# Kernel tuning notes

Hardware: AMD Instinct MI355X
Metric: run time of the kernel (lower is better)

## Reference

```python
import jax, jax.numpy as jnp
import numpy as np

B, S, E, H, L = 16, 1024, 512, 8, 4
D = E // H  # head_dim = 64


def setup_inputs() -> dict:
    key = jax.random.key(0)
    ks = jax.random.split(key, 16)
    std = 0.02
    inp = {
        "q": jax.random.normal(ks[0], (B, S, E), jnp.float32),
        "k": jax.random.normal(ks[1], (B, S, E), jnp.float32),
        "v": jax.random.normal(ks[2], (B, S, E), jnp.float32),
        # standard Linear params (torch convention: W is (out, in))
        "Wq": jax.random.normal(ks[3], (E, E), jnp.float32) * std,
        "bq": jnp.zeros((E,), jnp.float32),
        "Wk": jax.random.normal(ks[4], (E, E), jnp.float32) * std,
        "bk": jnp.zeros((E,), jnp.float32),
        # WFLinear: shared weight elementwise-multiplied by per-language factor
        "Wv_share": jax.random.normal(ks[5], (E, E), jnp.float32) * std,
        "Wv_spec": 1.0 + jax.random.normal(ks[6], (L, E, E), jnp.float32) * std,
        "bv_share": jnp.zeros((E,), jnp.float32),
        "bv_spec": jax.random.normal(ks[7], (L, E), jnp.float32) * std,
        "Wo_share": jax.random.normal(ks[8], (E, E), jnp.float32) * std,
        "Wo_spec": 1.0 + jax.random.normal(ks[9], (L, E, E), jnp.float32) * std,
        "bo_share": jnp.zeros((E,), jnp.float32),
        "bo_spec": jax.random.normal(ks[10], (L, E), jnp.float32) * std,
        "mask": jax.random.randint(ks[11], (B, S), 0, 2, jnp.int32),
        "languageID": 1,
    }
    return inp


def reference(q, k, v, Wq, bq, Wk, bk, Wv_share, Wv_spec, bv_share, bv_spec,
              Wo_share, Wo_spec, bo_share, bo_spec, mask, languageID):
    scaling = D ** (-0.5)
    # projections (torch Linear: x @ W.T + b)
    Q = (q @ Wq.T + bq).reshape(B, S, H, D).transpose(0, 2, 1, 3) * scaling
    K = (k @ Wk.T + bk).reshape(B, S, H, D).transpose(0, 2, 1, 3)
    Wv = Wv_share * Wv_spec[languageID]
    bv = bv_share + bv_spec[languageID]
    V = (v @ Wv.T + bv).reshape(B, S, H, D).transpose(0, 2, 1, 3)
    # NOTE: faithful to original — Q already scaled by d_k^-0.5, and
    # AttentionWF divides by sqrt(d_k) AGAIN (effective scale 1/d_k).
    alpha = jnp.einsum("bhqd,bhkd->bhqk", Q, K) / np.float32(np.sqrt(D))
    m = (mask == 0)[:, None, None, :]  # (B,1,1,S) over key axis
    alpha = jnp.where(m, jnp.float32(-1e9), alpha)
    alpha = jax.nn.softmax(alpha, axis=-1)
    # dropout p=0.0 -> identity
    ctx = jnp.einsum("bhqk,bhkd->bhqd", alpha, V)  # (B,H,S,D)
    concat = ctx.transpose(0, 2, 1, 3).reshape(B, S, E)
    Wo = Wo_share * Wo_spec[languageID]
    bo = bo_share + bo_spec[languageID]
    return concat @ Wo.T + bo
```

## Files before the change

### kernel.cpp

```cpp
#include <hip/hip_runtime.h>

#define B_ 16
#define S_ 1024
#define E_ 512
#define H_ 8
#define D_ 64
#define L_ 4
#define M_ (B_*S_)

typedef unsigned short u16;
typedef __attribute__((ext_vector_type(8))) short bf16x8;
typedef __attribute__((ext_vector_type(4))) float f32x4;
typedef __attribute__((ext_vector_type(4))) unsigned uint4v;

__device__ __forceinline__ u16 f2bf(float x) {
  unsigned u = __float_as_uint(x);
  unsigned r = (u + 0x7fffu + ((u >> 16) & 1u)) >> 16;
  return (u16)r;
}
__device__ __forceinline__ ushort4 f2bf4(float4 f) {
  ushort4 u;
  u.x = f2bf(f.x); u.y = f2bf(f.y); u.z = f2bf(f.z); u.w = f2bf(f.w);
  return u;
}
__device__ __forceinline__ unsigned cvt_pk_bf16(float lo, float hi) {
  unsigned r;
  asm("v_cvt_pk_bf16_f32 %0, %1, %2" : "=v"(r) : "v"(lo), "v"(hi));
  return r;
}

typedef __attribute__((address_space(1))) const void gconst_void;
typedef __attribute__((address_space(3))) void lds_void;
__device__ __forceinline__ void gl_lds16(const void* g, void* l) {
  __builtin_amdgcn_global_load_lds((gconst_void*)g, (lds_void*)l, 16, 0, 0);
}
__device__ __forceinline__ void fence_vm0_barrier() {
  asm volatile("s_waitcnt vmcnt(0)" ::: "memory");
  __builtin_amdgcn_s_barrier();
}

__global__ __launch_bounds__(256) void prep_w(
    const float* __restrict__ Wq, const float* __restrict__ Wk,
    const float* __restrict__ Wv_sh, const float* __restrict__ Wv_sp,
    const float* __restrict__ Wo_sh, const float* __restrict__ Wo_sp,
    const float* __restrict__ bv_sh, const float* __restrict__ bv_sp,
    const float* __restrict__ bo_sh, const float* __restrict__ bo_sp,
    const int* __restrict__ langp,
    u16* __restrict__ Wq_b, u16* __restrict__ Wk_b,
    u16* __restrict__ Wv_b, u16* __restrict__ Wo_b,
    float* __restrict__ bv_f, float* __restrict__ bo_f) {
  int lang = langp[0];
  int i = blockIdx.x * 256 + threadIdx.x;
  size_t wofs = (size_t)lang * (E_*E_/4) + i;
  ((ushort4*)Wq_b)[i] = f2bf4(((const float4*)Wq)[i]);
  ((ushort4*)Wk_b)[i] = f2bf4(((const float4*)Wk)[i]);
  float4 vs = ((const float4*)Wv_sh)[i], vp = ((const float4*)Wv_sp)[wofs];
  float4 os = ((const float4*)Wo_sh)[i], op = ((const float4*)Wo_sp)[wofs];
  float4 vv = {vs.x*vp.x, vs.y*vp.y, vs.z*vp.z, vs.w*vp.w};
  float4 oo = {os.x*op.x, os.y*op.y, os.z*op.z, os.w*op.w};
  ((ushort4*)Wv_b)[i] = f2bf4(vv);
  ((ushort4*)Wo_b)[i] = f2bf4(oo);
  if (i < E_/4) {
    float4 b1 = ((const float4*)bv_sh)[i], b2 = ((const float4*)(bv_sp + (size_t)lang*E_))[i];
    float4 b3 = ((const float4*)bo_sh)[i], b4 = ((const float4*)(bo_sp + (size_t)lang*E_))[i];
    float4 r1 = {b1.x+b2.x, b1.y+b2.y, b1.z+b2.z, b1.w+b2.w};
    float4 r2 = {b3.x+b4.x, b3.y+b4.y, b3.z+b4.z, b3.w+b4.w};
    ((float4*)bv_f)[i] = r1;
    ((float4*)bo_f)[i] = r2;
  }
}

#define QBUF 4096
__global__ __launch_bounds__(256) void gemm_qkv(
    const float* __restrict__ q, const float* __restrict__ k, const float* __restrict__ v,
    const u16* __restrict__ Wq_b, const u16* __restrict__ Wk_b, const u16* __restrict__ Wv_b,
    const float* __restrict__ bq, const float* __restrict__ bk, const float* __restrict__ bv,
    u16* __restrict__ Qb, u16* __restrict__ Kb, u16* __restrict__ Vt) {
  __shared__ __align__(16) float sAfD[2*QBUF];
  __shared__ __align__(16) u16   sBD[2*QBUF];
  const int z = blockIdx.y;
  const float* A    = (z == 0) ? q : (z == 1) ? k : v;
  const u16*   Bw   = (z == 0) ? Wq_b : (z == 1) ? Wk_b : Wv_b;
  const float* bias = (z == 0) ? bq : (z == 1) ? bk : bv;
  const int t = threadIdx.x;
  const int hw = blockIdx.x;
  const int wk = (hw & 7) * 64 + (hw >> 3);
  const int m0 = (wk >> 2) * 128, n0 = (wk & 3) * 128;
  const int lane = t & 63, wid = t >> 6;
  const int m16 = lane & 15, qq = lane >> 4;
  const int wrow = (wid >> 1) * 64, wcol = (wid & 1) * 64;
  f32x4 acc[4][4] = {};
  const int ca0 = wid*4;
  const float* ap[4];
#pragma unroll
  for (int i = 0; i < 4; ++i)
    ap[i] = A + (size_t)(m0 + (ca0+i)*8 + (lane >> 3)) * E_ + (lane & 7) * 4;
  const int cb0 = wid*2, cb1 = wid*2 + 1;
  const u16* bp0 = Bw + (size_t)(n0 + cb0*16 + (lane >> 2)) * E_ + (lane & 3) * 8;
  const u16* bp1 = Bw + (size_t)(n0 + cb1*16 + (lane >> 2)) * E_ + (lane & 3) * 8;
  {
#pragma unroll
    for (int i = 0; i < 4; ++i) gl_lds16(ap[i], &sAfD[(ca0+i)*256]);
    gl_lds16(bp0, &sBD[cb0*512]);
    gl_lds16(bp1, &sBD[cb1*512]);
#pragma unroll
    for (int i = 0; i < 4; ++i) ap[i] += 32;
    bp0 += 32; bp1 += 32;
  }
  fence_vm0_barrier();
  for (int kt = 0; kt < 16; ++kt) {
    if (kt < 15) {
      float* sa = &sAfD[((kt+1)&1)*QBUF];
      u16*   sb = &sBD[((kt+1)&1)*QBUF];
#pragma unroll
      for (int i = 0; i < 4; ++i) gl_lds16(ap[i], sa + (ca0+i)*256);
      gl_lds16(bp0, sb + cb0*512);
      gl_lds16(bp1, sb + cb1*512);
#pragma unroll
      for (int i = 0; i < 4; ++i) ap[i] += 32;
      bp0 += 32; bp1 += 32;
    }
    const float* saf = &sAfD[(kt&1)*QBUF];
    const u16*   sbb = &sBD[(kt&1)*QBUF];
    bf16x8 af[4], bfm[4];
#pragma unroll
    for (int mt = 0; mt < 4; ++mt) {
      const float* ar = saf + (wrow + mt*16 + m16) * 32 + qq*8;
      f32x4 a0 = *(const f32x4*)ar;
      f32x4 a1 = *(const f32x4*)(ar + 4);
      union { uint4v u; bf16x8 h; } cv;
      cv.u = (uint4v){ cvt_pk_bf16(a0[0], a0[1]), cvt_pk_bf16(a0[2], a0[3]),
                       cvt_pk_bf16(a1[0], a1[1]), cvt_pk_bf16(a1[2], a1[3]) };
      af[mt] = cv.h;
    }
#pragma unroll
    for (int nt = 0; nt < 4; ++nt)
      bfm[nt] = *(const bf16x8*)(sbb + (wcol + nt*16 + m16) * 32 + qq*8);
#pragma unroll
    for (int mt = 0; mt < 4; ++mt)
#pragma unroll
      for (int nt = 0; nt < 4; ++nt)
        acc[mt][nt] = __builtin_amdgcn_mfma_f32_16x16x32_bf16(af[mt], bfm[nt], acc[mt][nt], 0, 0, 0);
    if (kt < 15) fence_vm0_barrier();
  }
  float bvv[4];
#pragma unroll
  for (int nt = 0; nt < 4; ++nt) bvv[nt] = bias[n0 + wcol + nt*16 + m16];
  if (z < 2) {
    u16* out = (z == 0) ? Qb : Kb;
#pragma unroll
    for (int mt = 0; mt < 4; ++mt) {
      int gm = m0 + wrow + mt*16 + qq*4;
#pragma unroll
      for (int nt = 0; nt < 4; ++nt) {
        int gn = n0 + wcol + nt*16 + m16;
#pragma unroll
        for (int r = 0; r < 4; ++r)
          out[(size_t)(gm + r) * E_ + gn] = f2bf(acc[mt][nt][r] + bvv[nt]);
      }
    }
  } else {
#pragma unroll
    for (int mt = 0; mt < 4; ++mt) {
      int tok0 = m0 + wrow + mt*16 + qq*4;
      int bb = tok0 >> 10, s0 = tok0 & 1023;
#pragma unroll
      for (int nt = 0; nt < 4; ++nt) {
        int dim = n0 + wcol + nt*16 + m16;
        uint2 wv = { cvt_pk_bf16(acc[mt][nt][0] + bvv[nt], acc[mt][nt][1] + bvv[nt]),
                     cvt_pk_bf16(acc[mt][nt][2] + bvv[nt], acc[mt][nt][3] + bvv[nt]) };
        *(uint2*)(Vt + ((size_t)(bb*E_ + dim))*S_ + s0) = wv;
      }
    }
  }
}

__global__ __launch_bounds__(256) void gemm_lds(
    const u16* __restrict__ A, const u16* __restrict__ Bw,
    const float* __restrict__ bias, float* __restrict__ out) {
  __shared__ __align__(16) u16 sAD[2*QBUF];
  __shared__ __align__(16) u16 sBD[2*QBUF];
  const int t = threadIdx.x;
  const int hw = blockIdx.x;
  const int wk = (hw & 7) * 64 + (hw >> 3);
  const int m0 = (wk >> 2) * 128, n0 = (wk & 3) * 128;
  const int lane = t & 63, wid = t >> 6;
  const int m16 = lane & 15, qq = lane >> 4;
  const int wrow = (wid >> 1) * 64, wcol = (wid & 1) * 64;
  f32x4 acc[4][4] = {};
  const int c0 = 2*wid, c1 = 2*wid + 1;
  const int colk = (lane & 3) * 8;
  const int r0 = c0*16 + (lane >> 2), r1 = c1*16 + (lane >> 2);
  const u16* a0 = A  + (size_t)(m0 + r0) * E_ + colk;
  const u16* a1 = A  + (size_t)(m0 + r1) * E_ + colk;
  const u16* b0 = Bw + (size_t)(n0 + r0) * E_ + colk;
  const u16* b1 = Bw + (size_t)(n0 + r1) * E_ + colk;
  gl_lds16(a0, &sAD[c0*512]);
  gl_lds16(a1, &sAD[c1*512]);
  gl_lds16(b0, &sBD[c0*512]);
  gl_lds16(b1, &sBD[c1*512]);
  a0 += 32; a1 += 32; b0 += 32; b1 += 32;
  fence_vm0_barrier();
  for (int kt = 0; kt < 16; ++kt) {
    if (kt < 15) {
      u16* sa = &sAD[((kt+1)&1)*QBUF];
      u16* sb = &sBD[((kt+1)&1)*QBUF];
      gl_lds16(a0, sa + c0*512);
      gl_lds16(a1, sa + c1*512);
      gl_lds16(b0, sb + c0*512);
      gl_lds16(b1, sb + c1*512);
      a0 += 32; a1 += 32; b0 += 32; b1 += 32;
    }
    const u16* sa = &sAD[(kt&1)*QBUF];
    const u16* sb = &sBD[(kt&1)*QBUF];
    bf16x8 af[4], bfm[4];
#pragma unroll
    for (int mt = 0; mt < 4; ++mt)
      af[mt] = *(const bf16x8*)(sa + (wrow + mt*16 + m16) * 32 + qq*8);
#pragma unroll
    for (int nt = 0; nt < 4; ++nt)
      bfm[nt] = *(const bf16x8*)(sb + (wcol + nt*16 + m16) * 32 + qq*8);
#pragma unroll
    for (int mt = 0; mt < 4; ++mt)
#pragma unroll
      for (int nt = 0; nt < 4; ++nt)
        acc[mt][nt] = __builtin_amdgcn_mfma_f32_16x16x32_bf16(af[mt], bfm[nt], acc[mt][nt], 0, 0, 0);
    if (kt < 15) fence_vm0_barrier();
  }
  float bv[4];
#pragma unroll
  for (int nt = 0; nt < 4; ++nt) bv[nt] = bias[n0 + wcol + nt*16 + m16];
#pragma unroll
  for (int mt = 0; mt < 4; ++mt) {
    int gm = m0 + wrow + mt*16 + qq*4;
#pragma unroll
    for (int nt = 0; nt < 4; ++nt) {
      int gn = n0 + wcol + nt*16 + m16;
#pragma unroll
      for (int r = 0; r < 4; ++r)
        out[(size_t)(gm + r) * E_ + gn] = acc[mt][nt][r] + bv[nt];
    }
  }
}

#define KST 72
__global__ __launch_bounds__(256) void attn_mfma(
    const u16* __restrict__ Qb, const u16* __restrict__ Kb, const u16* __restrict__ Vt,
    const int* __restrict__ mask, u16* __restrict__ ctxb) {
  __shared__ __align__(16) u16 sK[64*KST];
  __shared__ __align__(16) u16 sV[64*KST];
  __shared__ __align__(16) u16 sP[64*KST];
  __shared__ __align__(16) float sMask[64];
  __shared__ __align__(16) float sL[64];
  const int t = threadIdx.x;
  const int lane = t & 63, w = t >> 6;
  const int m16 = lane & 15, quad = lane >> 4;
  const int hw = blockIdx.x;
  const int wk = (hw & 7) * 256 + (hw >> 3);
  const int bh = wk >> 4, b = bh >> 3, h = bh & 7;
  const int qblk = (wk & 15) * 64;
  const int q0 = qblk + w * 16;
  bf16x8 qf0, qf1;
  {
    const u16* qp = Qb + (size_t)(b*S_ + q0 + m16) * E_ + h*D_ + quad*8;
    qf0 = *(const bf16x8*)qp;
    qf1 = *(const bf16x8*)(qp + 32);
  }
  f32x4 oacc[4] = {};
  float lpart = 0.f;
  const int srow = t >> 2, sc0 = (t & 3) * 16;
  const u16* kp = Kb + (size_t)(b*S_ + srow) * E_ + h*D_ + sc0;
  const u16* vp = Vt + ((size_t)(b*H_ + h) * D_ + srow) * S_ + sc0;
  uint4 rk0 = *(const uint4*)kp, rk1 = *(const uint4*)(kp + 8);
  uint4 rv0 = *(const uint4*)vp, rv1 = *(const uint4*)(vp + 8);
  float rmsk = 0.f;
  if (t < 64) rmsk = (mask[b*S_ + t] == 0) ? -1e9f : 0.f;
  const float CS = 0.015625f * 1.44269504f;
  for (int kt = 0; kt < S_; kt += 64) {
    *(uint4*)&sK[srow*KST + sc0]     = rk0;
    *(uint4*)&sK[srow*KST + sc0 + 8] = rk1;
    *(uint4*)&sV[srow*KST + sc0]     = rv0;
    *(uint4*)&sV[srow*KST + sc0 + 8] = rv1;
    if (t < 64) sMask[t] = rmsk;
    __syncthreads();
    if (kt + 64 < S_) {
      kp += (size_t)64 * E_; vp += 64;
      rk0 = *(const uint4*)kp; rk1 = *(const uint4*)(kp + 8);
      rv0 = *(const uint4*)vp; rv1 = *(const uint4*)(vp + 8);
      if (t < 64) rmsk = (mask[b*S_ + kt + 64 + t] == 0) ? -1e9f : 0.f;
    }
    f32x4 sacc[4] = {};
#pragma unroll
    for (int ct = 0; ct < 4; ++ct) {
      bf16x8 kf0 = *(const bf16x8*)&sK[(ct*16 + m16)*KST + quad*8];
      bf16x8 kf1 = *(const bf16x8*)&sK[(ct*16 + m16)*KST + 32 + quad*8];
      sacc[ct] = __builtin_amdgcn_mfma_f32_16x16x32_bf16(kf0, qf0, sacc[ct], 0, 0, 0);
      sacc[ct] = __builtin_amdgcn_mfma_f32_16x16x32_bf16(kf1, qf1, sacc[ct], 0, 0, 0);
    }
#pragma unroll
    for (int ct = 0; ct < 4; ++ct) {
      f32x4 msk = *(const f32x4*)&sMask[ct*16 + quad*4];
      float p0 = exp2f(fmaf(sacc[ct][0], CS, msk[0]));
      float p1 = exp2f(fmaf(sacc[ct][1], CS, msk[1]));
      float p2 = exp2f(fmaf(sacc[ct][2], CS, msk[2]));
      float p3 = exp2f(fmaf(sacc[ct][3], CS, msk[3]));
      lpart += (p0 + p1) + (p2 + p3);
      uint2 pq = { cvt_pk_bf16(p0, p1), cvt_pk_bf16(p2, p3) };
      *(uint2*)&sP[(w*16 + m16)*KST + ct*16 + quad*4] = pq;
    }
    bf16x8 pf0 = *(const bf16x8*)&sP[(w*16 + m16)*KST + quad*8];
    bf16x8 pf1 = *(const bf16x8*)&sP[(w*16 + m16)*KST + 32 + quad*8];
#pragma unroll
    for (int dt = 0; dt < 4; ++dt) {
      bf16x8 vf0 = *(const bf16x8*)&sV[(dt*16 + m16)*KST + quad*8];
      bf16x8 vf1 = *(const bf16x8*)&sV[(dt*16 + m16)*KST + 32 + quad*8];
      oacc[dt] = __builtin_amdgcn_mfma_f32_16x16x32_bf16(pf0, vf0, oacc[dt], 0, 0, 0);
      oacc[dt] = __builtin_amdgcn_mfma_f32_16x16x32_bf16(pf1, vf1, oacc[dt], 0, 0, 0);
    }
    __syncthreads();
  }
  lpart += __shfl_xor(lpart, 16);
  lpart += __shfl_xor(lpart, 32);
  if (quad == 0) sL[w*16 + m16] = lpart;
  float inv[4];
#pragma unroll
  for (int r = 0; r < 4; ++r) inv[r] = 1.0f / sL[w*16 + quad*4 + r];
#pragma unroll
  for (int dt = 0; dt < 4; ++dt)
#pragma unroll
    for (int r = 0; r < 4; ++r)
      sP[(w*16 + quad*4 + r)*KST + dt*16 + m16] = f2bf(oacc[dt][r] * inv[r]);
  __syncthreads();
  const int orow = t >> 2, oc0 = (t & 3) * 16;
  uint4 o0 = *(uint4*)&sP[orow*KST + oc0];
  uint4 o1 = *(uint4*)&sP[orow*KST + oc0 + 8];
  u16* dst = ctxb + (size_t)(b*S_ + qblk + orow) * E_ + h*D_ + oc0;
  *(uint4*)dst = o0;
  *(uint4*)(dst + 8) = o1;
}

extern "C" void kernel_launch(void* const* d_in, const int* in_sizes, int n_in,
                              void* d_out, int out_size, void* d_ws, size_t ws_size,
                              hipStream_t stream) {
  const float* q     = (const float*)d_in[0];
  const float* k     = (const float*)d_in[1];
  const float* v     = (const float*)d_in[2];
  const float* Wq    = (const float*)d_in[3];
  const float* bq    = (const float*)d_in[4];
  const float* Wk    = (const float*)d_in[5];
  const float* bk    = (const float*)d_in[6];
  const float* Wv_sh = (const float*)d_in[7];
  const float* Wv_sp = (const float*)d_in[8];
  const float* bv_sh = (const float*)d_in[9];
  const float* bv_sp = (const float*)d_in[10];
  const float* Wo_sh = (const float*)d_in[11];
  const float* Wo_sp = (const float*)d_in[12];
  const float* bo_sh = (const float*)d_in[13];
  const float* bo_sp = (const float*)d_in[14];
  const int*   mask  = (const int*)d_in[15];
  const int*   lang  = (const int*)d_in[16];

  char* ws = (char*)d_ws;
  size_t off = 0;
  auto alloc = [&](size_t bytes) -> char* {
    char* p = ws + off;
    off += (bytes + 255) & ~(size_t)255;
    return p;
  };
  u16* Qb   = (u16*)alloc((size_t)M_ * E_ * 2);
  u16* Kb   = (u16*)alloc((size_t)M_ * E_ * 2);
  u16* Vt   = (u16*)alloc((size_t)M_ * E_ * 2);
  u16* ctxb = (u16*)alloc((size_t)M_ * E_ * 2);
  u16* Wq_b = (u16*)alloc((size_t)E_ * E_ * 2);
  u16* Wk_b = (u16*)alloc((size_t)E_ * E_ * 2);
  u16* Wv_b = (u16*)alloc((size_t)E_ * E_ * 2);
  u16* Wo_b = (u16*)alloc((size_t)E_ * E_ * 2);
  float* bv_f = (float*)alloc(E_ * 4);
  float* bo_f = (float*)alloc(E_ * 4);

  prep_w<<<E_*E_/1024, 256, 0, stream>>>(Wq, Wk, Wv_sh, Wv_sp, Wo_sh, Wo_sp,
                                         bv_sh, bv_sp, bo_sh, bo_sp, lang,
                                         Wq_b, Wk_b, Wv_b, Wo_b, bv_f, bo_f);

  dim3 qkvgrid(512, 3);
  gemm_qkv<<<qkvgrid, 256, 0, stream>>>(q, k, v, Wq_b, Wk_b, Wv_b,
                                        bq, bk, bv_f, Qb, Kb, Vt);

  attn_mfma<<<2048, 256, 0, stream>>>(Qb, Kb, Vt, mask, ctxb);

  gemm_lds<<<512, 256, 0, stream>>>(ctxb, Wo_b, bo_f, (float*)d_out);
}
```

Before: 309.9 us.

## Convert QKV activations to bf16 before LDS, swizzle LDS, retile output GEMM

The QKV GEMM now loads fp32 activations into registers, converts them to bf16, and stores them in an XOR-swizzled LDS layout. This halves LDS footprint and avoids repeating the conversion for every MFMA read. The B operand loads in both GEMMs are remapped so the swizzled layout avoids bank conflicts, and launch bounds request 4 blocks per CU. The output GEMM moves to 128x64 tiles with twice as many blocks, raising occupancy and parallelism at the cost of reloading the A tile more often.

```diff
diff --git a/kernel.cpp b/kernel.cpp
--- a/kernel.cpp
+++ b/kernel.cpp
@@ -38,6 +38,7 @@
   asm volatile("s_waitcnt vmcnt(0)" ::: "memory");
   __builtin_amdgcn_s_barrier();
 }
+
 
 __global__ __launch_bounds__(256) void prep_w(
     const float* __restrict__ Wq, const float* __restrict__ Wk,
@@ -70,14 +71,14 @@
   }
 }
 
-#define QBUF 4096
-__global__ __launch_bounds__(256) void gemm_qkv(
+#define ABBUF 8192
+__global__ __launch_bounds__(256, 4) void gemm_qkv(
     const float* __restrict__ q, const float* __restrict__ k, const float* __restrict__ v,
     const u16* __restrict__ Wq_b, const u16* __restrict__ Wk_b, const u16* __restrict__ Wv_b,
     const float* __restrict__ bq, const float* __restrict__ bk, const float* __restrict__ bv,
     u16* __restrict__ Qb, u16* __restrict__ Kb, u16* __restrict__ Vt) {
-  __shared__ __align__(16) float sAfD[2*QBUF];
-  __shared__ __align__(16) u16   sBD[2*QBUF];
+  __shared__ __align__(16) u16 sA[2*4096];
+  __shared__ __align__(16) u16 sB[2*4096];
   const int z = blockIdx.y;
   const float* A    = (z == 0) ? q : (z == 1) ? k : v;
   const u16*   Bw   = (z == 0) ? Wq_b : (z == 1) ? Wk_b : Wv_b;
@@ -89,59 +90,77 @@
   const int lane = t & 63, wid = t >> 6;
   const int m16 = lane & 15, qq = lane >> 4;
   const int wrow = (wid >> 1) * 64, wcol = (wid & 1) * 64;
+  const int key = (lane & 7) << 4;
   f32x4 acc[4][4] = {};
-  const int ca0 = wid*4;
-  const float* ap[4];
-#pragma unroll
-  for (int i = 0; i < 4; ++i)
-    ap[i] = A + (size_t)(m0 + (ca0+i)*8 + (lane >> 3)) * E_ + (lane & 7) * 4;
+  const int arow = t >> 1;
+  const float* aR = A + (size_t)(m0 + arow) * E_ + (t & 1) * 16;
+  const int awr0 = (arow*64 + (t&1)*32)      ^ ((arow & 7) << 4);
+  const int awr1 = (arow*64 + (t&1)*32 + 16) ^ ((arow & 7) << 4);
   const int cb0 = wid*2, cb1 = wid*2 + 1;
-  const u16* bp0 = Bw + (size_t)(n0 + cb0*16 + (lane >> 2)) * E_ + (lane & 3) * 8;
-  const u16* bp1 = Bw + (size_t)(n0 + cb1*16 + (lane >> 2)) * E_ + (lane & 3) * 8;
+  const int rl0 = ((lane>>2)&1) ^ ((lane>>4)&1);
+  const int brow = 2*(lane>>3) + rl0;
+  const int bcol = (((lane&1)^rl0)<<3) + ((((lane>>1)&1) ^ ((lane>>3)&1))<<4);
+  const u16* bp0 = Bw + (size_t)(n0 + cb0*16 + brow) * E_ + bcol;
+  const u16* bp1 = Bw + (size_t)(n0 + cb1*16 + brow) * E_ + bcol;
+  char* sAb = (char*)sA;
+  char* sBb = (char*)sB;
+  gl_lds16(bp0, sBb + cb0*1024);
+  gl_lds16(bp1, sBb + cb1*1024);
+  f32x4 ar0 = *(const f32x4*)aR;
+  f32x4 ar1 = *(const f32x4*)(aR + 4);
+  f32x4 ar2 = *(const f32x4*)(aR + 8);
+  f32x4 ar3 = *(const f32x4*)(aR + 12);
+  aR += 32; bp0 += 32; bp1 += 32;
+  asm volatile("s_waitcnt vmcnt(0)" ::: "memory");
   {
-#pragma unroll
-    for (int i = 0; i < 4; ++i) gl_lds16(ap[i], &sAfD[(ca0+i)*256]);
-    gl_lds16(bp0, &sBD[cb0*512]);
-    gl_lds16(bp1, &sBD[cb1*512]);
-#pragma unroll
-    for (int i = 0; i < 4; ++i) ap[i] += 32;
-    bp0 += 32; bp1 += 32;
-  }
-  fence_vm0_barrier();
+    uint4v w0 = { cvt_pk_bf16(ar0[0],ar0[1]), cvt_pk_bf16(ar0[2],ar0[3]),
+                  cvt_pk_bf16(ar1[0],ar1[1]), cvt_pk_bf16(ar1[2],ar1[3]) };
+    uint4v w1 = { cvt_pk_bf16(ar2[0],ar2[1]), cvt_pk_bf16(ar2[2],ar2[3]),
+                  cvt_pk_bf16(ar3[0],ar3[1]), cvt_pk_bf16(ar3[2],ar3[3]) };
+    *(uint4v*)(sAb + awr0) = w0;
+    *(uint4v*)(sAb + awr1) = w1;
+  }
+  asm volatile("s_waitcnt lgkmcnt(0)" ::: "memory");
+  __builtin_amdgcn_s_barrier();
   for (int kt = 0; kt < 16; ++kt) {
+    const int cur = (kt & 1) * ABBUF;
+    const int nxt = ABBUF - cur;
     if (kt < 15) {
-      float* sa = &sAfD[((kt+1)&1)*QBUF];
-      u16*   sb = &sBD[((kt+1)&1)*QBUF];
-#pragma unroll
-      for (int i = 0; i < 4; ++i) gl_lds16(ap[i], sa + (ca0+i)*256);
-      gl_lds16(bp0, sb + cb0*512);
-      gl_lds16(bp1, sb + cb1*512);
-#pragma unroll
-      for (int i = 0; i < 4; ++i) ap[i] += 32;
-      bp0 += 32; bp1 += 32;
-    }
-    const float* saf = &sAfD[(kt&1)*QBUF];
-    const u16*   sbb = &sBD[(kt&1)*QBUF];
+      gl_lds16(bp0, sBb + nxt + cb0*1024);
+      gl_lds16(bp1, sBb + nxt + cb1*1024);
+      ar0 = *(const f32x4*)aR;
+      ar1 = *(const f32x4*)(aR + 4);
+      ar2 = *(const f32x4*)(aR + 8);
+      ar3 = *(const f32x4*)(aR + 12);
+      aR += 32; bp0 += 32; bp1 += 32;
+    }
     bf16x8 af[4], bfm[4];
 #pragma unroll
     for (int mt = 0; mt < 4; ++mt) {
-      const float* ar = saf + (wrow + mt*16 + m16) * 32 + qq*8;
-      f32x4 a0 = *(const f32x4*)ar;
-      f32x4 a1 = *(const f32x4*)(ar + 4);
-      union { uint4v u; bf16x8 h; } cv;
-      cv.u = (uint4v){ cvt_pk_bf16(a0[0], a0[1]), cvt_pk_bf16(a0[2], a0[3]),
-                       cvt_pk_bf16(a1[0], a1[1]), cvt_pk_bf16(a1[2], a1[3]) };
-      af[mt] = cv.h;
-    }
-#pragma unroll
-    for (int nt = 0; nt < 4; ++nt)
-      bfm[nt] = *(const bf16x8*)(sbb + (wcol + nt*16 + m16) * 32 + qq*8);
+      int row = wrow + mt*16 + m16;
+      af[mt] = *(const bf16x8*)(sAb + cur + ((row*64 + qq*16) ^ key));
+    }
+#pragma unroll
+    for (int nt = 0; nt < 4; ++nt) {
+      int row = wcol + nt*16 + m16;
+      bfm[nt] = *(const bf16x8*)(sBb + cur + ((row*64 + qq*16) ^ key));
+    }
 #pragma unroll
     for (int mt = 0; mt < 4; ++mt)
 #pragma unroll
       for (int nt = 0; nt < 4; ++nt)
         acc[mt][nt] = __builtin_amdgcn_mfma_f32_16x16x32_bf16(af[mt], bfm[nt], acc[mt][nt], 0, 0, 0);
-    if (kt < 15) fence_vm0_barrier();
+    if (kt < 15) {
+      asm volatile("s_waitcnt vmcnt(0)" ::: "memory");
+      uint4v w0 = { cvt_pk_bf16(ar0[0],ar0[1]), cvt_pk_bf16(ar0[2],ar0[3]),
+                    cvt_pk_bf16(ar1[0],ar1[1]), cvt_pk_bf16(ar1[2],ar1[3]) };
+      uint4v w1 = { cvt_pk_bf16(ar2[0],ar2[1]), cvt_pk_bf16(ar2[2],ar2[3]),
+                    cvt_pk_bf16(ar3[0],ar3[1]), cvt_pk_bf16(ar3[2],ar3[3]) };
+      *(uint4v*)(sAb + nxt + awr0) = w0;
+      *(uint4v*)(sAb + nxt + awr1) = w1;
+      asm volatile("s_waitcnt lgkmcnt(0)" ::: "memory");
+      __builtin_amdgcn_s_barrier();
+    }
   }
   float bvv[4];
 #pragma unroll
@@ -175,66 +194,69 @@
   }
 }
 
-__global__ __launch_bounds__(256) void gemm_lds(
+__global__ __launch_bounds__(256, 4) void gemm_lds(
     const u16* __restrict__ A, const u16* __restrict__ Bw,
     const float* __restrict__ bias, float* __restrict__ out) {
-  __shared__ __align__(16) u16 sAD[2*QBUF];
-  __shared__ __align__(16) u16 sBD[2*QBUF];
+  __shared__ __align__(16) u16 sAD[2*4096];
+  __shared__ __align__(16) u16 sBD[2*2048];
   const int t = threadIdx.x;
   const int hw = blockIdx.x;
-  const int wk = (hw & 7) * 64 + (hw >> 3);
-  const int m0 = (wk >> 2) * 128, n0 = (wk & 3) * 128;
+  const int wk = (hw & 7) * 128 + (hw >> 3);
+  const int m0 = (wk >> 3) * 128, n0 = (wk & 7) * 64;
   const int lane = t & 63, wid = t >> 6;
   const int m16 = lane & 15, qq = lane >> 4;
-  const int wrow = (wid >> 1) * 64, wcol = (wid & 1) * 64;
-  f32x4 acc[4][4] = {};
+  const int wrow = (wid >> 1) * 64, wcol = (wid & 1) * 32;
+  const int key = (lane & 7) << 4;
+  f32x4 acc[4][2] = {};
+  const int rl0 = ((lane>>2)&1) ^ ((lane>>4)&1);
+  const int brow = 2*(lane>>3) + rl0;
+  const int bcol = (((lane&1)^rl0)<<3) + ((((lane>>1)&1) ^ ((lane>>3)&1))<<4);
   const int c0 = 2*wid, c1 = 2*wid + 1;
-  const int colk = (lane & 3) * 8;
-  const int r0 = c0*16 + (lane >> 2), r1 = c1*16 + (lane >> 2);
-  const u16* a0 = A  + (size_t)(m0 + r0) * E_ + colk;
-  const u16* a1 = A  + (size_t)(m0 + r1) * E_ + colk;
-  const u16* b0 = Bw + (size_t)(n0 + r0) * E_ + colk;
-  const u16* b1 = Bw + (size_t)(n0 + r1) * E_ + colk;
-  gl_lds16(a0, &sAD[c0*512]);
-  gl_lds16(a1, &sAD[c1*512]);
-  gl_lds16(b0, &sBD[c0*512]);
-  gl_lds16(b1, &sBD[c1*512]);
-  a0 += 32; a1 += 32; b0 += 32; b1 += 32;
+  const u16* a0 = A  + (size_t)(m0 + c0*16 + brow) * E_ + bcol;
+  const u16* a1 = A  + (size_t)(m0 + c1*16 + brow) * E_ + bcol;
+  const u16* b0 = Bw + (size_t)(n0 + wid*16 + brow) * E_ + bcol;
+  char* sAb = (char*)sAD;
+  char* sBb = (char*)sBD;
+  gl_lds16(a0, sAb + c0*1024);
+  gl_lds16(a1, sAb + c1*1024);
+  gl_lds16(b0, sBb + wid*1024);
+  a0 += 32; a1 += 32; b0 += 32;
   fence_vm0_barrier();
   for (int kt = 0; kt < 16; ++kt) {
+    const int curA = (kt & 1) * 8192, nxtA = 8192 - curA;
+    const int curB = (kt & 1) * 4096, nxtB = 4096 - curB;
     if (kt < 15) {
-      u16* sa = &sAD[((kt+1)&1)*QBUF];
-      u16* sb = &sBD[((kt+1)&1)*QBUF];
-      gl_lds16(a0, sa + c0*512);
-      gl_lds16(a1, sa + c1*512);
-      gl_lds16(b0, sb + c0*512);
-      gl_lds16(b1, sb + c1*512);
-      a0 += 32; a1 += 32; b0 += 32; b1 += 32;
-    }
-    const u16* sa = &sAD[(kt&1)*QBUF];
-    const u16* sb = &sBD[(kt&1)*QBUF];
-    bf16x8 af[4], bfm[4];
+      gl_lds16(a0, sAb + nxtA + c0*1024);
+      gl_lds16(a1, sAb + nxtA + c1*1024);
+      gl_lds16(b0, sBb + nxtB + wid*1024);
+      a0 += 32; a1 += 32; b0 += 32;
+    }
+    bf16x8 af[4], bfm[2];
+#pragma unroll
+    for (int mt = 0; mt < 4; ++mt) {
+      int row = wrow + mt*16 + m16;
+      af[mt] = *(const bf16x8*)(sAb + curA + ((row*64 + qq*16) ^ key));
+    }
+#pragma unroll
+    for (int nt = 0; nt < 2; ++nt) {
+      int row = wcol + nt*16 + m16;
+      bfm[nt] = *(const bf16x8*)(sBb + curB + ((row*64 + qq*16) ^ key));
+    }
 #pragma unroll
     for (int mt = 0; mt < 4; ++mt)
-      af[mt] = *(const bf16x8*)(sa + (wrow + mt*16 + m16) * 32 + qq*8);
-#pragma unroll
-    for (int nt = 0; nt < 4; ++nt)
-      bfm[nt] = *(const bf16x8*)(sb + (wcol + nt*16 + m16) * 32 + qq*8);
-#pragma unroll
-    for (int mt = 0; mt < 4; ++mt)
-#pragma unroll
-      for (int nt = 0; nt < 4; ++nt)
+#pragma unroll
+      for (int nt = 0; nt < 2; ++nt)
         acc[mt][nt] = __builtin_amdgcn_mfma_f32_16x16x32_bf16(af[mt], bfm[nt], acc[mt][nt], 0, 0, 0);
     if (kt < 15) fence_vm0_barrier();
   }
-  float bv[4];
-#pragma unroll
-  for (int nt = 0; nt < 4; ++nt) bv[nt] = bias[n0 + wcol + nt*16 + m16];
+  float bv[2];
+#pragma unroll
+  for (int nt = 0; nt < 2; ++nt) bv[nt] = bias[n0 + wcol + nt*16 + m16];
 #pragma unroll
   for (int mt = 0; mt < 4; ++mt) {
     int gm = m0 + wrow + mt*16 + qq*4;
 #pragma unroll
-    for (int nt = 0; nt < 4; ++nt) {
+    for (int nt = 0; nt < 2; ++nt) {
       int gn = n0 + wcol + nt*16 + m16;
 #pragma unroll
       for (int r = 0; r < 4; ++r)
@@ -388,5 +410,5 @@
 
   attn_mfma<<<2048, 256, 0, stream>>>(Qb, Kb, Vt, mask, ctxb);
 
-  gemm_lds<<<512, 256, 0, stream>>>(ctxb, Wo_b, bo_f, (float*)d_out);
-}
+  gemm_lds<<<1024, 256, 0, stream>>>(ctxb, Wo_b, bo_f, (float*)d_out);
+}
```

New measurement: 302.0 us. -2.6%, faster.
